# Performance work log

Hardware: AMD Instinct MI355X
Metric: run time of the kernel (lower is better)

Reference implementation:

```python
import jax, jax.numpy as jnp
import numpy as np

B, T, S, D = 4, 16, 256, 1024
H, HKV = 16, 4
HD = D // H  # 64
N_IMG = 240  # image tokens; remaining S-N_IMG are agent tokens
LOGIT_CAP = 50.0
EPS = 1e-6


def _build_mask():
    # modality-aware mask: image tokens see only image tokens; agent tokens see all
    m = np.zeros((S, S), dtype=bool)
    m[:N_IMG, :N_IMG] = True
    m[N_IMG:, :] = True
    return jnp.asarray(m)


def _build_rope(s, hd):
    half = hd // 2
    inv_freq = 1.0 / (10000.0 ** (np.arange(half, dtype=np.float32) / half))
    pos = np.arange(s, dtype=np.float32)
    ang = np.outer(pos, inv_freq)  # (S, hd/2)
    return jnp.asarray(np.cos(ang)), jnp.asarray(np.sin(ang))


def setup_inputs() -> dict:
    key = jax.random.key(0)
    ks = jax.random.split(key, 7)
    rope_cos, rope_sin = _build_rope(S, HD)
    sc = 0.02
    return {
        "x": jax.random.normal(ks[0], (B, T, S, D), jnp.float32),
        "attn_mask": _build_mask(),
        "rope_cos": rope_cos,
        "rope_sin": rope_sin,
        "Wq": jax.random.normal(ks[1], (D, H * HD), jnp.float32) * sc,
        "Wk": jax.random.normal(ks[2], (D, HKV * HD), jnp.float32) * sc,
        "Wv": jax.random.normal(ks[3], (D, HKV * HD), jnp.float32) * sc,
        "Wo": jax.random.normal(ks[4], (D, D), jnp.float32) * sc,
        "q_scale": jnp.ones((HD,), jnp.float32),
        "k_scale": jnp.ones((HD,), jnp.float32),
    }


def _rmsnorm(t, scale):
    # RMSNorm over head_dim
    var = jnp.mean(jnp.square(t), axis=-1, keepdims=True)
    return t * jax.lax.rsqrt(var + EPS) * scale


def _rope(t, cos, sin):
    # rotate-half RoPE; t: (N, S, h, hd), cos/sin: (S, hd/2)
    half = t.shape[-1] // 2
    t1, t2 = t[..., :half], t[..., half:]
    c = cos[None, :, None, :]
    s = sin[None, :, None, :]
    return jnp.concatenate([t1 * c - t2 * s, t2 * c + t1 * s], axis=-1)


def reference(x, attn_mask, rope_cos, rope_sin, Wq, Wk, Wv, Wo, q_scale, k_scale):
    b, t, s, d = x.shape
    n = b * t
    xf = x.reshape(n, s, d)
    q = (xf @ Wq).reshape(n, s, H, HD)
    k = (xf @ Wk).reshape(n, s, HKV, HD)
    v = (xf @ Wv).reshape(n, s, HKV, HD)
    # QK-norm then RoPE
    q = _rope(_rmsnorm(q, q_scale), rope_cos, rope_sin)
    k = _rope(_rmsnorm(k, k_scale), rope_cos, rope_sin)
    # GQA: repeat kv heads
    rep = H // HKV
    k = jnp.repeat(k, rep, axis=2)
    v = jnp.repeat(v, rep, axis=2)
    scale = 1.0 / jnp.sqrt(jnp.asarray(HD, x.dtype))
    scores = jnp.einsum('nqhd,nkhd->nhqk', q, k) * scale
    # logit soft-capping
    scores = LOGIT_CAP * jnp.tanh(scores / LOGIT_CAP)
    big_neg = jnp.asarray(jnp.finfo(scores.dtype).min, scores.dtype)
    scores = jnp.where(attn_mask[None, None], scores, big_neg)
    p = jax.nn.softmax(scores, axis=-1)
    out = jnp.einsum('nhqk,nkhd->nqhd', p, v).reshape(n, s, d)
    return (out @ Wo).reshape(b, t, s, d)
```

## Files before the change

### kernel.cpp

```cpp
#include <hip/hip_runtime.h>

typedef __bf16 v8bf __attribute__((ext_vector_type(8)));
typedef __bf16 v4bf __attribute__((ext_vector_type(4)));
typedef float floatx4 __attribute__((ext_vector_type(4)));

#define MFMA16(a, b, c) __builtin_amdgcn_mfma_f32_16x16x32_bf16(a, b, c, 0, 0, 0)
#define GLL16(gp, lp)                                                        \
    __builtin_amdgcn_global_load_lds(                                        \
        (const __attribute__((address_space(1))) void*)(gp),                 \
        (__attribute__((address_space(3))) void*)(lp), 16, 0, 0)

__global__ void cast_x(const float* __restrict__ x, __bf16* __restrict__ xb, int n4) {
    int i = blockIdx.x * blockDim.x + threadIdx.x;
    int stride = gridDim.x * blockDim.x;
    for (; i < n4; i += stride) {
        float4 v = ((const float4*)x)[i];
        v4bf o;
        o[0] = (__bf16)v.x; o[1] = (__bf16)v.y; o[2] = (__bf16)v.z; o[3] = (__bf16)v.w;
        ((v4bf*)xb)[i] = o;
    }
}

__global__ void transW(const float* __restrict__ W0, const float* __restrict__ W1,
                       const float* __restrict__ W2, __bf16* __restrict__ dst) {
    __shared__ __bf16 tile[64][65];
    int k0 = blockIdx.x * 64, c0 = blockIdx.y * 64;
    for (int i = threadIdx.x; i < 4096; i += 256) {
        int k = i >> 6, c = i & 63;
        int gc = c0 + c;
        float v;
        if (gc < 1024)      v = W0[(k0 + k) * 1024 + gc];
        else if (gc < 1280) v = W1[(k0 + k) * 256 + gc - 1024];
        else                v = W2[(k0 + k) * 256 + gc - 1280];
        tile[c][k] = (__bf16)v;
    }
    __syncthreads();
    for (int i = threadIdx.x; i < 4096; i += 256) {
        int c = i >> 6, k = i & 63;
        dst[(c0 + c) * 1024 + k0 + k] = tile[c][k];
    }
}

__global__ __launch_bounds__(256) void gemm_bt(const __bf16* __restrict__ A,
                                               const __bf16* __restrict__ B,
                                               __bf16* __restrict__ Cb,
                                               float* __restrict__ Cf,
                                               int N, int K) {
    __shared__ __attribute__((aligned(16))) __bf16 As[128 * 32];
    __shared__ __attribute__((aligned(16))) __bf16 Bs[128 * 32];
    const int t = threadIdx.x, lane = t & 63, w = t >> 6;
    const int m0 = blockIdx.y * 128, n0 = blockIdx.x * 128;
    const int wm = (w >> 1) * 64, wn = (w & 1) * 64;
    const int rl = lane >> 2;
    const int gl = (lane & 3) ^ ((lane >> 3) & 3);
    const __bf16* pA0 = A + (long)(m0 + w * 16 + rl) * K + gl * 8;
    const __bf16* pA1 = A + (long)(m0 + 64 + w * 16 + rl) * K + gl * 8;
    const __bf16* pB0 = B + (long)(n0 + w * 16 + rl) * K + gl * 8;
    const __bf16* pB1 = B + (long)(n0 + 64 + w * 16 + rl) * K + gl * 8;
    __bf16* lA0 = &As[(w * 16) * 32];
    __bf16* lA1 = &As[(64 + w * 16) * 32];
    __bf16* lB0 = &Bs[(w * 16) * 32];
    __bf16* lB1 = &Bs[(64 + w * 16) * 32];
    const int lr = lane & 15, quad = lane >> 4;
    const int ga = ((quad ^ ((lr >> 1) & 3)) * 8);
    floatx4 acc[4][4] = {};
    for (int kk = 0; kk < K; kk += 32) {
        __syncthreads();
        GLL16(pA0 + kk, lA0);
        GLL16(pA1 + kk, lA1);
        GLL16(pB0 + kk, lB0);
        GLL16(pB1 + kk, lB1);
        __syncthreads();
        v8bf af[4], bq[4];
#pragma unroll
        for (int i = 0; i < 4; ++i) af[i] = *(const v8bf*)(&As[(wm + i * 16 + lr) * 32 + ga]);
#pragma unroll
        for (int j = 0; j < 4; ++j) bq[j] = *(const v8bf*)(&Bs[(wn + j * 16 + lr) * 32 + ga]);
#pragma unroll
        for (int i = 0; i < 4; ++i)
#pragma unroll
            for (int j = 0; j < 4; ++j)
                acc[i][j] = MFMA16(af[i], bq[j], acc[i][j]);
    }
#pragma unroll
    for (int i = 0; i < 4; ++i)
#pragma unroll
        for (int j = 0; j < 4; ++j)
#pragma unroll
            for (int r = 0; r < 4; ++r) {
                int row = m0 + wm + i * 16 + (lane >> 4) * 4 + r;
                int col = n0 + wn + j * 16 + (lane & 15);
                if (Cf) Cf[(long)row * N + col] = acc[i][j][r];
                else    Cb[(long)row * N + col] = (__bf16)acc[i][j][r];
            }
}

__global__ __launch_bounds__(256) void qknorm(const __bf16* __restrict__ qkv,
                                              const float* __restrict__ rc,
                                              const float* __restrict__ rs,
                                              const float* __restrict__ qsc,
                                              const float* __restrict__ ksc,
                                              __bf16* __restrict__ Q,
                                              __bf16* __restrict__ Kb) {
    int item = blockIdx.x * 4 + (threadIdx.x >> 6);
    int lane = threadIdx.x & 63;
    int row, col0, s;
    const float* scale;
    __bf16* dst;
    if (item < 262144) {
        row = item >> 4;
        int h = item & 15;
        int n = row >> 8; s = row & 255;
        col0 = h * 64; scale = qsc;
        dst = Q + ((long)((n * 16 + h) * 256) + s) * 64;
    } else {
        int j = item - 262144;
        row = j >> 2;
        int hk = j & 3;
        int n = row >> 8; s = row & 255;
        col0 = 1024 + hk * 64; scale = ksc;
        dst = Kb + ((long)((n * 4 + hk) * 256) + s) * 64;
    }
    float v = (float)qkv[(long)row * 1536 + col0 + lane];
    float sq = v * v;
#pragma unroll
    for (int msk = 1; msk < 64; msk <<= 1) sq += __shfl_xor(sq, msk);
    float rr = rsqrtf(sq * (1.f / 64.f) + 1e-6f);
    v = v * rr * scale[lane];
    float c = rc[s * 32 + (lane & 31)];
    float sn = rs[s * 32 + (lane & 31)];
    float p = __shfl_xor(v, 32);
    v = (lane < 32) ? (v * c - p * sn) : (v * c + p * sn);
    dst[lane] = (__bf16)v;
}

__global__ __launch_bounds__(512) void attn_kernel(const __bf16* __restrict__ Q,
                                                   const __bf16* __restrict__ Kb,
                                                   const __bf16* __restrict__ qkv,
                                                   __bf16* __restrict__ O) {
    __shared__ __attribute__((aligned(16))) __bf16 KV[256 * 64];
    __shared__ __attribute__((aligned(16))) __bf16 Ps[8][16][40];
    const int bx = blockIdx.x;
    const int n = bx >> 5, h = (bx >> 1) & 15, half = bx & 1, hk = h >> 2;
    const int t = threadIdx.x, lane = t & 63, w = t >> 6;
    const int m = lane & 15, quad = lane >> 4;

    for (int p = 0; p < 4; ++p) {
        int l = t + p * 512;
        int s = l >> 3, cg = l & 7;
        v8bf kv = *(const v8bf*)(Kb + ((long)((n * 4 + hk) * 256 + s) << 6) + cg * 8);
        *(v8bf*)(&KV[s * 64 + ((cg ^ (s & 7)) * 8)]) = kv;
    }
    const __bf16* qp = Q + ((long)((n * 16 + h) * 256 + half * 128 + w * 16 + m) << 6) + quad * 8;
    v8bf qa0 = *(const v8bf*)(qp);
    v8bf qa1 = *(const v8bf*)(qp + 32);
    __syncthreads();

    floatx4 sc[16];
#pragma unroll
    for (int ti = 0; ti < 16; ++ti) {
        int srow = ti * 16 + m;
        v8bf b0 = *(const v8bf*)(&KV[srow * 64 + ((quad ^ (srow & 7)) * 8)]);
        v8bf b1 = *(const v8bf*)(&KV[srow * 64 + (((quad + 4) ^ (srow & 7)) * 8)]);
        floatx4 a = {0.f, 0.f, 0.f, 0.f};
        a = MFMA16(qa0, b0, a);
        a = MFMA16(qa1, b1, a);
        sc[ti] = a;
    }

    const int qbase = half * 128 + w * 16 + quad * 4;
    float sum[4] = {0.f, 0.f, 0.f, 0.f};
#pragma unroll
    for (int ti = 0; ti < 16; ++ti)
#pragma unroll
        for (int r = 0; r < 4; ++r) {
            float v = sc[ti][r];
            float e = __builtin_amdgcn_exp2f(v * 0.0072134752f);
            float capped = 50.f - 100.f * __builtin_amdgcn_rcpf(e + 1.f);
            float p = __builtin_amdgcn_exp2f(capped * 1.44269504f);
            if (ti == 15 && (qbase + r) < 240) p = 0.f;
            sc[ti][r] = p;
            sum[r] += p;
        }
    float inv[4];
#pragma unroll
    for (int r = 0; r < 4; ++r) {
#pragma unroll
        for (int msk = 1; msk < 16; msk <<= 1) sum[r] += __shfl_xor(sum[r], msk);
        inv[r] = __builtin_amdgcn_rcpf(sum[r]);
    }

    __syncthreads();
    for (int p = 0; p < 4; ++p) {
        int l = t + p * 512;
        int s = l >> 3, cg = l & 7;
        v8bf vv = *(const v8bf*)(qkv + (long)(n * 256 + s) * 1536 + 1280 + hk * 64 + cg * 8);
#pragma unroll
        for (int j = 0; j < 8; ++j)
            KV[(cg * 8 + j) * 256 + ((s >> 3) ^ j) * 8 + (s & 7)] = vv[j];
    }
    __syncthreads();

    floatx4 oacc[4] = {};
#pragma unroll
    for (int kc = 0; kc < 8; ++kc) {
#pragma unroll
        for (int ht = 0; ht < 2; ++ht) {
            int ti = kc * 2 + ht;
#pragma unroll
            for (int r = 0; r < 4; ++r)
                Ps[w][quad * 4 + r][ht * 16 + m] = (__bf16)sc[ti][r];
        }
        v8bf pa = *(const v8bf*)(&Ps[w][m][quad * 8]);
#pragma unroll
        for (int ct = 0; ct < 4; ++ct) {
            int hd = ct * 16 + m;
            int sg = kc * 4 + quad;
            v8bf vb = *(const v8bf*)(&KV[hd * 256 + ((sg ^ (hd & 7)) * 8)]);
            oacc[ct] = MFMA16(pa, vb, oacc[ct]);
        }
    }
#pragma unroll
    for (int ct = 0; ct < 4; ++ct)
#pragma unroll
        for (int r = 0; r < 4; ++r) {
            int qrow = half * 128 + w * 16 + quad * 4 + r;
            O[(long)(n * 256 + qrow) * 1024 + h * 64 + ct * 16 + m] =
                (__bf16)(oacc[ct][r] * inv[r]);
        }
}

extern "C" void kernel_launch(void* const* d_in, const int* in_sizes, int n_in,
                              void* d_out, int out_size, void* d_ws, size_t ws_size,
                              hipStream_t stream) {
    const float* x  = (const float*)d_in[0];
    const float* rc = (const float*)d_in[2];
    const float* rs = (const float*)d_in[3];
    const float* Wq = (const float*)d_in[4];
    const float* Wk = (const float*)d_in[5];
    const float* Wv = (const float*)d_in[6];
    const float* Wo = (const float*)d_in[7];
    const float* qs = (const float*)d_in[8];
    const float* ks = (const float*)d_in[9];
    float* out = (float*)d_out;
    char* ws = (char*)d_ws;

    __bf16* x_bf    = (__bf16*)(ws);
    __bf16* WqkvT   = (__bf16*)(ws + 33554432);
    __bf16* WoT     = (__bf16*)(ws + 36700160);
    __bf16* qkv_bf  = (__bf16*)(ws + 38797312);
    __bf16* K_bf    = (__bf16*)(ws + 89128960);
    __bf16* attn_bf = (__bf16*)(ws + 97517568);
    __bf16* Q_bf    = x_bf;

    cast_x<<<4096, 256, 0, stream>>>(x, x_bf, 16777216 / 4);
    transW<<<dim3(16, 24), 256, 0, stream>>>(Wq, Wk, Wv, WqkvT);
    transW<<<dim3(16, 16), 256, 0, stream>>>(Wo, Wo, Wo, WoT);
    gemm_bt<<<dim3(12, 128), 256, 0, stream>>>(x_bf, WqkvT, qkv_bf, nullptr, 1536, 1024);
    qknorm<<<81920, 256, 0, stream>>>(qkv_bf, rc, rs, qs, ks, Q_bf, K_bf);
    attn_kernel<<<2048, 512, 0, stream>>>(Q_bf, K_bf, qkv_bf, attn_bf);
    gemm_bt<<<dim3(8, 128), 256, 0, stream>>>(attn_bf, WoT, nullptr, out, 1024, 1024);
}
```

Before: 377.0 us.

## Fuse QK RMSNorm and RoPE into QKV GEMM epilogue, vectorize GEMM stores

Folds the separate qknorm kernel into the QKV GEMM epilogue. Each 64-column warp tile is one head, so the RMSNorm reduction and RoPE rotation run on the accumulators before they are written straight into head-major Q/K and a compact V buffer. Both GEMM epilogues now stage results through LDS to issue 16-byte coalesced stores, and the two weight transposes are merged into one launch. This removes the round trip of the full qkv intermediate and two kernel launches, at the cost of extra epilogue register pressure and LDS traffic.

New measurement: 349.7 us. 7.2% less time.

```diff
diff --git a/kernel.cpp b/kernel.cpp
--- a/kernel.cpp
+++ b/kernel.cpp
@@ -22,49 +22,60 @@
 }
 
 __global__ void transW(const float* __restrict__ W0, const float* __restrict__ W1,
-                       const float* __restrict__ W2, __bf16* __restrict__ dst) {
+                       const float* __restrict__ W2, const float* __restrict__ W3,
+                       __bf16* __restrict__ dqkv, __bf16* __restrict__ dwo) {
     __shared__ __bf16 tile[64][65];
-    int k0 = blockIdx.x * 64, c0 = blockIdx.y * 64;
+    int k0 = blockIdx.x * 64;
+    int byy = blockIdx.y;
+    bool isO = byy >= 24;
+    int c0 = (isO ? byy - 24 : byy) * 64;
     for (int i = threadIdx.x; i < 4096; i += 256) {
         int k = i >> 6, c = i & 63;
         int gc = c0 + c;
         float v;
-        if (gc < 1024)      v = W0[(k0 + k) * 1024 + gc];
+        if (isO)            v = W3[(k0 + k) * 1024 + gc];
+        else if (gc < 1024) v = W0[(k0 + k) * 1024 + gc];
         else if (gc < 1280) v = W1[(k0 + k) * 256 + gc - 1024];
         else                v = W2[(k0 + k) * 256 + gc - 1280];
         tile[c][k] = (__bf16)v;
     }
     __syncthreads();
+    __bf16* dst = isO ? dwo : dqkv;
     for (int i = threadIdx.x; i < 4096; i += 256) {
         int c = i >> 6, k = i & 63;
         dst[(c0 + c) * 1024 + k0 + k] = tile[c][k];
     }
 }
 
-__global__ __launch_bounds__(256) void gemm_bt(const __bf16* __restrict__ A,
-                                               const __bf16* __restrict__ B,
-                                               __bf16* __restrict__ Cb,
-                                               float* __restrict__ Cf,
-                                               int N, int K) {
-    __shared__ __attribute__((aligned(16))) __bf16 As[128 * 32];
-    __shared__ __attribute__((aligned(16))) __bf16 Bs[128 * 32];
+__global__ __launch_bounds__(256) void gemm_qkv(const __bf16* __restrict__ A,
+                                                const __bf16* __restrict__ B,
+                                                const float* __restrict__ rc,
+                                                const float* __restrict__ rs,
+                                                const float* __restrict__ qsc,
+                                                const float* __restrict__ ksc,
+                                                __bf16* __restrict__ Q,
+                                                __bf16* __restrict__ Kb,
+                                                __bf16* __restrict__ V) {
+    __shared__ __attribute__((aligned(16))) __bf16 smem[8192];
+    __bf16* As = smem;
+    __bf16* Bs = smem + 4096;
     const int t = threadIdx.x, lane = t & 63, w = t >> 6;
     const int m0 = blockIdx.y * 128, n0 = blockIdx.x * 128;
     const int wm = (w >> 1) * 64, wn = (w & 1) * 64;
     const int rl = lane >> 2;
     const int gl = (lane & 3) ^ ((lane >> 3) & 3);
-    const __bf16* pA0 = A + (long)(m0 + w * 16 + rl) * K + gl * 8;
-    const __bf16* pA1 = A + (long)(m0 + 64 + w * 16 + rl) * K + gl * 8;
-    const __bf16* pB0 = B + (long)(n0 + w * 16 + rl) * K + gl * 8;
-    const __bf16* pB1 = B + (long)(n0 + 64 + w * 16 + rl) * K + gl * 8;
+    const __bf16* pA0 = A + (long)(m0 + w * 16 + rl) * 1024 + gl * 8;
+    const __bf16* pA1 = A + (long)(m0 + 64 + w * 16 + rl) * 1024 + gl * 8;
+    const __bf16* pB0 = B + (long)(n0 + w * 16 + rl) * 1024 + gl * 8;
+    const __bf16* pB1 = B + (long)(n0 + 64 + w * 16 + rl) * 1024 + gl * 8;
     __bf16* lA0 = &As[(w * 16) * 32];
     __bf16* lA1 = &As[(64 + w * 16) * 32];
     __bf16* lB0 = &Bs[(w * 16) * 32];
     __bf16* lB1 = &Bs[(64 + w * 16) * 32];
-    const int lr = lane & 15, quad = lane >> 4;
+    const int lr = lane & 15, quad = lane >> 4, m = lane & 15;
     const int ga = ((quad ^ ((lr >> 1) & 3)) * 8);
     floatx4 acc[4][4] = {};
-    for (int kk = 0; kk < K; kk += 32) {
+    for (int kk = 0; kk < 1024; kk += 32) {
         __syncthreads();
         GLL16(pA0 + kk, lA0);
         GLL16(pA1 + kk, lA1);
@@ -82,61 +93,133 @@
             for (int j = 0; j < 4; ++j)
                 acc[i][j] = MFMA16(af[i], bq[j], acc[i][j]);
     }
-#pragma unroll
-    for (int i = 0; i < 4; ++i)
+    __syncthreads();
+    const int bx = blockIdx.x;
+    const int n = m0 >> 8;
+    __bf16* tile = smem + w * (16 * 68);
+    const int row2 = lane >> 2, cb = lane & 3;
+    float scl[4] = {0.f, 0.f, 0.f, 0.f};
+    if (bx < 10) {
+        const float* sc = (bx < 8) ? qsc : ksc;
+#pragma unroll
+        for (int j = 0; j < 4; ++j) scl[j] = sc[j * 16 + m];
+    }
+#pragma unroll
+    for (int i = 0; i < 4; ++i) {
+        float vals[4][4];
+        if (bx < 10) {
+#pragma unroll
+            for (int r = 0; r < 4; ++r) {
+                float ss = 0.f;
+#pragma unroll
+                for (int j = 0; j < 4; ++j) ss += acc[i][j][r] * acc[i][j][r];
+                ss += __shfl_xor(ss, 1); ss += __shfl_xor(ss, 2);
+                ss += __shfl_xor(ss, 4); ss += __shfl_xor(ss, 8);
+                float rr = rsqrtf(ss * (1.f / 64.f) + 1e-6f);
+                int s = (m0 & 255) + wm + i * 16 + quad * 4 + r;
+                float c0v = rc[s * 32 + m],      c1v = rc[s * 32 + 16 + m];
+                float s0v = rs[s * 32 + m],      s1v = rs[s * 32 + 16 + m];
+                float v0 = acc[i][0][r] * rr * scl[0];
+                float v1 = acc[i][1][r] * rr * scl[1];
+                float v2 = acc[i][2][r] * rr * scl[2];
+                float v3 = acc[i][3][r] * rr * scl[3];
+                vals[0][r] = v0 * c0v - v2 * s0v;
+                vals[1][r] = v1 * c1v - v3 * s1v;
+                vals[2][r] = v2 * c0v + v0 * s0v;
+                vals[3][r] = v3 * c1v + v1 * s1v;
+            }
+        } else {
+#pragma unroll
+            for (int j = 0; j < 4; ++j)
+#pragma unroll
+                for (int r = 0; r < 4; ++r) vals[j][r] = acc[i][j][r];
+        }
 #pragma unroll
         for (int j = 0; j < 4; ++j)
 #pragma unroll
-            for (int r = 0; r < 4; ++r) {
-                int row = m0 + wm + i * 16 + (lane >> 4) * 4 + r;
-                int col = n0 + wn + j * 16 + (lane & 15);
-                if (Cf) Cf[(long)row * N + col] = acc[i][j][r];
-                else    Cb[(long)row * N + col] = (__bf16)acc[i][j][r];
-            }
-}
-
-__global__ __launch_bounds__(256) void qknorm(const __bf16* __restrict__ qkv,
-                                              const float* __restrict__ rc,
-                                              const float* __restrict__ rs,
-                                              const float* __restrict__ qsc,
-                                              const float* __restrict__ ksc,
-                                              __bf16* __restrict__ Q,
-                                              __bf16* __restrict__ Kb) {
-    int item = blockIdx.x * 4 + (threadIdx.x >> 6);
-    int lane = threadIdx.x & 63;
-    int row, col0, s;
-    const float* scale;
-    __bf16* dst;
-    if (item < 262144) {
-        row = item >> 4;
-        int h = item & 15;
-        int n = row >> 8; s = row & 255;
-        col0 = h * 64; scale = qsc;
-        dst = Q + ((long)((n * 16 + h) * 256) + s) * 64;
-    } else {
-        int j = item - 262144;
-        row = j >> 2;
-        int hk = j & 3;
-        int n = row >> 8; s = row & 255;
-        col0 = 1024 + hk * 64; scale = ksc;
-        dst = Kb + ((long)((n * 4 + hk) * 256) + s) * 64;
-    }
-    float v = (float)qkv[(long)row * 1536 + col0 + lane];
-    float sq = v * v;
-#pragma unroll
-    for (int msk = 1; msk < 64; msk <<= 1) sq += __shfl_xor(sq, msk);
-    float rr = rsqrtf(sq * (1.f / 64.f) + 1e-6f);
-    v = v * rr * scale[lane];
-    float c = rc[s * 32 + (lane & 31)];
-    float sn = rs[s * 32 + (lane & 31)];
-    float p = __shfl_xor(v, 32);
-    v = (lane < 32) ? (v * c - p * sn) : (v * c + p * sn);
-    dst[lane] = (__bf16)v;
+            for (int r = 0; r < 4; ++r)
+                tile[(quad * 4 + r) * 68 + j * 16 + m] = (__bf16)vals[j][r];
+        v8bf o0 = *(const v8bf*)(&tile[row2 * 68 + cb * 16]);
+        v8bf o1 = *(const v8bf*)(&tile[row2 * 68 + cb * 16 + 8]);
+        int s = (m0 & 255) + wm + i * 16 + row2;
+        __bf16* dst;
+        if (bx < 8) {
+            int h = bx * 2 + (w & 1);
+            dst = Q + (((long)((n * 16 + h) * 256 + s)) << 6) + cb * 16;
+        } else if (bx < 10) {
+            int hk = (bx - 8) * 2 + (w & 1);
+            dst = Kb + (((long)((n * 4 + hk) * 256 + s)) << 6) + cb * 16;
+        } else {
+            int vc = (bx - 10) * 128 + wn + cb * 16;
+            dst = V + (((long)(n * 256 + s)) << 8) + vc;
+        }
+        *(v8bf*)dst = o0;
+        *(v8bf*)(dst + 8) = o1;
+    }
+}
+
+__global__ __launch_bounds__(256) void gemm_o(const __bf16* __restrict__ A,
+                                              const __bf16* __restrict__ B,
+                                              float* __restrict__ Cf) {
+    __shared__ __attribute__((aligned(16))) __bf16 smem[8448];
+    __bf16* As = smem;
+    __bf16* Bs = smem + 4096;
+    const int t = threadIdx.x, lane = t & 63, w = t >> 6;
+    const int m0 = blockIdx.y * 128, n0 = blockIdx.x * 128;
+    const int wm = (w >> 1) * 64, wn = (w & 1) * 64;
+    const int rl = lane >> 2;
+    const int gl = (lane & 3) ^ ((lane >> 3) & 3);
+    const __bf16* pA0 = A + (long)(m0 + w * 16 + rl) * 1024 + gl * 8;
+    const __bf16* pA1 = A + (long)(m0 + 64 + w * 16 + rl) * 1024 + gl * 8;
+    const __bf16* pB0 = B + (long)(n0 + w * 16 + rl) * 1024 + gl * 8;
+    const __bf16* pB1 = B + (long)(n0 + 64 + w * 16 + rl) * 1024 + gl * 8;
+    __bf16* lA0 = &As[(w * 16) * 32];
+    __bf16* lA1 = &As[(64 + w * 16) * 32];
+    __bf16* lB0 = &Bs[(w * 16) * 32];
+    __bf16* lB1 = &Bs[(64 + w * 16) * 32];
+    const int lr = lane & 15, quad = lane >> 4, m = lane & 15;
+    const int ga = ((quad ^ ((lr >> 1) & 3)) * 8);
+    floatx4 acc[4][4] = {};
+    for (int kk = 0; kk < 1024; kk += 32) {
+        __syncthreads();
+        GLL16(pA0 + kk, lA0);
+        GLL16(pA1 + kk, lA1);
+        GLL16(pB0 + kk, lB0);
+        GLL16(pB1 + kk, lB1);
+        __syncthreads();
+        v8bf af[4], bq[4];
+#pragma unroll
+        for (int i = 0; i < 4; ++i) af[i] = *(const v8bf*)(&As[(wm + i * 16 + lr) * 32 + ga]);
+#pragma unroll
+        for (int j = 0; j < 4; ++j) bq[j] = *(const v8bf*)(&Bs[(wn + j * 16 + lr) * 32 + ga]);
+#pragma unroll
+        for (int i = 0; i < 4; ++i)
+#pragma unroll
+            for (int j = 0; j < 4; ++j)
+                acc[i][j] = MFMA16(af[i], bq[j], acc[i][j]);
+    }
+    __syncthreads();
+    float* tile = (float*)smem + w * (16 * 66);
+    const int row2 = lane >> 2, cb = lane & 3;
+#pragma unroll
+    for (int i = 0; i < 4; ++i) {
+#pragma unroll
+        for (int j = 0; j < 4; ++j)
+#pragma unroll
+            for (int r = 0; r < 4; ++r)
+                tile[(quad * 4 + r) * 66 + j * 16 + m] = acc[i][j][r];
+        float* dst = Cf + (long)(m0 + wm + i * 16 + row2) * 1024 + n0 + wn + cb * 16;
+#pragma unroll
+        for (int c = 0; c < 4; ++c) {
+            floatx4 o = *(const floatx4*)(&tile[row2 * 66 + cb * 16 + c * 4]);
+            *(floatx4*)(dst + c * 4) = o;
+        }
+    }
 }
 
 __global__ __launch_bounds__(512) void attn_kernel(const __bf16* __restrict__ Q,
                                                    const __bf16* __restrict__ Kb,
-                                                   const __bf16* __restrict__ qkv,
+                                                   const __bf16* __restrict__ Vb,
                                                    __bf16* __restrict__ O) {
     __shared__ __attribute__((aligned(16))) __bf16 KV[256 * 64];
     __shared__ __attribute__((aligned(16))) __bf16 Ps[8][16][40];
@@ -194,7 +277,7 @@
     for (int p = 0; p < 4; ++p) {
         int l = t + p * 512;
         int s = l >> 3, cg = l & 7;
-        v8bf vv = *(const v8bf*)(qkv + (long)(n * 256 + s) * 1536 + 1280 + hk * 64 + cg * 8);
+        v8bf vv = *(const v8bf*)(Vb + ((long)(n * 256 + s) << 8) + hk * 64 + cg * 8);
 #pragma unroll
         for (int j = 0; j < 8; ++j)
             KV[(cg * 8 + j) * 256 + ((s >> 3) ^ j) * 8 + (s & 7)] = vv[j];
@@ -246,18 +329,16 @@
     char* ws = (char*)d_ws;
 
     __bf16* x_bf    = (__bf16*)(ws);
-    __bf16* WqkvT   = (__bf16*)(ws + 33554432);
-    __bf16* WoT     = (__bf16*)(ws + 36700160);
-    __bf16* qkv_bf  = (__bf16*)(ws + 38797312);
-    __bf16* K_bf    = (__bf16*)(ws + 89128960);
-    __bf16* attn_bf = (__bf16*)(ws + 97517568);
-    __bf16* Q_bf    = x_bf;
+    __bf16* WqkvT   = (__bf16*)(ws + (32l << 20));
+    __bf16* WoT     = (__bf16*)(ws + (35l << 20));
+    __bf16* Q_bf    = (__bf16*)(ws + (37l << 20));
+    __bf16* K_bf    = (__bf16*)(ws + (69l << 20));
+    __bf16* V_bf    = (__bf16*)(ws + (77l << 20));
+    __bf16* attn_bf = (__bf16*)(ws + (85l << 20));
 
     cast_x<<<4096, 256, 0, stream>>>(x, x_bf, 16777216 / 4);
-    transW<<<dim3(16, 24), 256, 0, stream>>>(Wq, Wk, Wv, WqkvT);
-    transW<<<dim3(16, 16), 256, 0, stream>>>(Wo, Wo, Wo, WoT);
-    gemm_bt<<<dim3(12, 128), 256, 0, stream>>>(x_bf, WqkvT, qkv_bf, nullptr, 1536, 1024);
-    qknorm<<<81920, 256, 0, stream>>>(qkv_bf, rc, rs, qs, ks, Q_bf, K_bf);
-    attn_kernel<<<2048, 512, 0, stream>>>(Q_bf, K_bf, qkv_bf, attn_bf);
-    gemm_bt<<<dim3(8, 128), 256, 0, stream>>>(attn_bf, WoT, nullptr, out, 1024, 1024);
-}
+    transW<<<dim3(16, 40), 256, 0, stream>>>(Wq, Wk, Wv, Wo, WqkvT, WoT);
+    gemm_qkv<<<dim3(12, 128), 256, 0, stream>>>(x_bf, WqkvT, rc, rs, qs, ks, Q_bf, K_bf, V_bf);
+    attn_kernel<<<2048, 512, 0, stream>>>(Q_bf, K_bf, V_bf, attn_bf);
+    gemm_o<<<dim3(8, 128), 256, 0, stream>>>(attn_bf, WoT, out);
+}
```
